# Kernel optimization log

Hardware: AMD Instinct MI355X
Metric: run time of the kernel (lower is better)

Reference implementation:

```python
import jax, jax.numpy as jnp
import numpy as np

DIM = 768
HEADS = 12
HEAD_DIM = DIM // HEADS
HIDDEN = 4 * DIM
EPS = 1e-5


def layernorm(x, g, b):
    mu = jnp.mean(x, axis=-1, keepdims=True)
    var = jnp.var(x, axis=-1, keepdims=True)
    return (x - mu) * jax.lax.rsqrt(var + EPS) * g + b


def setup_inputs() -> dict:
    key = jax.random.key(0)
    ks = jax.random.split(key, 16)
    s = 0.02
    return {
        "x_pre": jax.random.normal(ks[0], (8, 512, DIM), jnp.float32),
        "x_post": jax.random.normal(ks[1], (8, 512, DIM), jnp.float32),
        "attention_mask": jnp.zeros((8, 1, 1024, 1024), jnp.float32),
        "ln1_g": jnp.ones((DIM,), jnp.float32),
        "ln1_b": jnp.zeros((DIM,), jnp.float32),
        "Wq": jax.random.normal(ks[2], (DIM, DIM), jnp.float32) * s,
        "bq": jnp.zeros((DIM,), jnp.float32),
        "Wk": jax.random.normal(ks[3], (DIM, DIM), jnp.float32) * s,
        "bk": jnp.zeros((DIM,), jnp.float32),
        "Wv": jax.random.normal(ks[4], (DIM, DIM), jnp.float32) * s,
        "bv": jnp.zeros((DIM,), jnp.float32),
        "Wo": jax.random.normal(ks[5], (DIM, DIM), jnp.float32) * s,
        "bo": jnp.zeros((DIM,), jnp.float32),
        "ln2_g": jnp.ones((DIM,), jnp.float32),
        "ln2_b": jnp.zeros((DIM,), jnp.float32),
        "W1": jax.random.normal(ks[6], (DIM, HIDDEN), jnp.float32) * s,
        "b1": jnp.zeros((HIDDEN,), jnp.float32),
        "W2": jax.random.normal(ks[7], (HIDDEN, DIM), jnp.float32) * s,
        "b2": jnp.zeros((DIM,), jnp.float32),
        "gamma_1": 0.1 * jnp.ones((DIM,), jnp.float32),
        "gamma_2": 0.1 * jnp.ones((DIM,), jnp.float32),
    }


def reference(x_pre, x_post, attention_mask, ln1_g, ln1_b, Wq, bq, Wk, bk, Wv, bv,
              Wo, bo, ln2_g, ln2_b, W1, b1, W2, b2, gamma_1, gamma_2):
    x = jnp.concatenate((x_pre, x_post), axis=1)  # [B, N, C]
    B, N, C = x.shape
    h = layernorm(x, ln1_g, ln1_b)
    # self-attention with manual QK^T in float32
    q = (h @ Wq + bq).reshape(B, N, HEADS, HEAD_DIM)
    k = (h @ Wk + bk).reshape(B, N, HEADS, HEAD_DIM)
    v = (h @ Wv + bv).reshape(B, N, HEADS, HEAD_DIM)
    scale = HEAD_DIM ** -0.5
    attn = jnp.einsum("bqhd,bkhd->bhqk", q.astype(jnp.float32) * scale,
                      k.astype(jnp.float32)) + attention_mask
    attn = jax.nn.softmax(attn, axis=-1).astype(x.dtype)
    o = jnp.einsum("bhqk,bkhd->bqhd", attn, v).reshape(B, N, C)
    o = o @ Wo + bo
    x = x + gamma_1 * o
    # MLP
    h2 = layernorm(x, ln2_g, ln2_b)
    h2 = jax.nn.gelu(h2 @ W1 + b1, approximate=False) @ W2 + b2
    return x + gamma_2 * h2
```

## Files before the change

kernel.cpp:

```cpp
#include <hip/hip_runtime.h>
#include <hip/hip_fp8.h>
#include <cstdint>
#include <cstddef>

#define BATCH   8
#define SEQ     1024
#define DIMC    768
#define HEADS   12
#define HDIM    64
#define HIDDEN  3072
#define MROWS   (BATCH * SEQ)
#define L2E     1.4426950408889634f

typedef __attribute__((ext_vector_type(8))) short bf16x8;
typedef __attribute__((ext_vector_type(4))) float f32x4;

__device__ __forceinline__ unsigned short f2b(float f) {
    union { float f; unsigned int u; } v; v.f = f;
    unsigned int u = v.u;
    return (unsigned short)((u + 0x7FFFu + ((u >> 16) & 1u)) >> 16);
}
__device__ __forceinline__ unsigned char f2e4m3(float f) {
    __hip_fp8_e4m3 t(f); return t.__x;
}
__device__ __forceinline__ unsigned int b2u(float f) {
    union { float f; unsigned int u; } v; v.f = f; return v.u;
}
__device__ __forceinline__ float u2f(unsigned int u) {
    union { unsigned int u; float f; } v; v.u = u; return v.f;
}
__device__ __forceinline__ void gl_lds16(const void* g, void* l) {
    __builtin_amdgcn_global_load_lds(
        (const __attribute__((address_space(1))) unsigned int*)g,
        (__attribute__((address_space(3))) unsigned int*)l, 16, 0, 0);
}
__device__ __forceinline__ float gelu_fast(float x) {
    float p = x * x;
    float a = fmaf(p, 0.044715f, 1.0f);
    float w = x * a * -2.302118131f;
    float z = exp2f(w);
    return x * __builtin_amdgcn_rcpf(1.0f + z);
}

__global__ __launch_bounds__(256) void tcvt_k(const float* __restrict__ src,
                                              unsigned char* __restrict__ dst,
                                              int K, int N) {
    __shared__ float tile[32][33];
    int k0 = blockIdx.y * 32, n0 = blockIdx.x * 32;
    int tx = threadIdx.x, ty = threadIdx.y;
#pragma unroll
    for (int i = 0; i < 4; i++)
        tile[ty + i * 8][tx] = src[(size_t)(k0 + ty + i * 8) * N + n0 + tx];
    __syncthreads();
#pragma unroll
    for (int i = 0; i < 4; i++)
        dst[(size_t)(n0 + ty + i * 8) * K + k0 + tx] = f2e4m3(tile[tx][ty + i * 8]);
}

__global__ __launch_bounds__(256) void tcvt4_k(const float* __restrict__ s0,
                                               const float* __restrict__ s1,
                                               const float* __restrict__ s2,
                                               const float* __restrict__ s3,
                                               unsigned char* __restrict__ d0,
                                               unsigned char* __restrict__ d1,
                                               unsigned char* __restrict__ d2,
                                               unsigned char* __restrict__ d3) {
    const float* src = (blockIdx.z == 0) ? s0 : (blockIdx.z == 1) ? s1
                     : (blockIdx.z == 2) ? s2 : s3;
    unsigned char* dst = (blockIdx.z == 0) ? d0 : (blockIdx.z == 1) ? d1
                       : (blockIdx.z == 2) ? d2 : d3;
    __shared__ float tile[32][33];
    int k0 = blockIdx.y * 32, n0 = blockIdx.x * 32;
    int tx = threadIdx.x, ty = threadIdx.y;
#pragma unroll
    for (int i = 0; i < 4; i++)
        tile[ty + i * 8][tx] = src[(size_t)(k0 + ty + i * 8) * DIMC + n0 + tx];
    __syncthreads();
#pragma unroll
    for (int i = 0; i < 4; i++)
        dst[(size_t)(n0 + ty + i * 8) * DIMC + k0 + tx] = f2e4m3(tile[tx][ty + i * 8]);
}

__global__ __launch_bounds__(256) void vtr_k(const unsigned short* __restrict__ src,
                                             unsigned char* __restrict__ dst) {
    int bh = blockIdx.x, k0 = blockIdx.y * 64;
    __shared__ unsigned short t[64][68];
    const unsigned short* s = src + ((size_t)bh * SEQ + k0) * HDIM;
    unsigned char* d = dst + (size_t)bh * HDIM * SEQ + k0;
    int tid = threadIdx.x;
#pragma unroll
    for (int p = 0; p < 4; p++) {
        int c = p * 256 + tid;
        int key = c >> 4, dd = (c & 15) * 4;
        *(uint2*)&t[key][dd] = *(const uint2*)&s[key * HDIM + dd];
    }
    __syncthreads();
#pragma unroll
    for (int p = 0; p < 8; p++) {
        int idx = p * 256 + tid;
        int dd = idx >> 5, kk = (idx & 31) * 2;
        uchar2 o;
        o.x = f2e4m3(u2f((unsigned int)t[kk][dd] << 16));
        o.y = f2e4m3(u2f((unsigned int)t[kk + 1][dd] << 16));
        *(uchar2*)&d[(size_t)dd * SEQ + kk] = o;
    }
}

__global__ __launch_bounds__(256) void ln_k(const float* __restrict__ xa,
                                            const float* __restrict__ xb,
                                            const float* __restrict__ g,
                                            const float* __restrict__ bt,
                                            float* __restrict__ x_out,
                                            unsigned char* __restrict__ h_out) {
    int r = blockIdx.x;
    const float* src;
    if (xb) {
        int b = r >> 10, nn = r & 1023;
        src = (nn < 512) ? xa + ((size_t)b * 512 + nn) * DIMC
                         : xb + ((size_t)b * 512 + (nn - 512)) * DIMC;
    } else {
        src = xa + (size_t)r * DIMC;
    }
    int t = threadIdx.x;
    float v[3], s = 0.f, s2 = 0.f;
#pragma unroll
    for (int j = 0; j < 3; j++) {
        v[j] = src[t + j * 256];
        s += v[j]; s2 += v[j] * v[j];
    }
#pragma unroll
    for (int off = 32; off > 0; off >>= 1) {
        s  += __shfl_down(s,  off);
        s2 += __shfl_down(s2, off);
    }
    __shared__ float red[8];
    int wid = t >> 6, lane = t & 63;
    if (lane == 0) { red[wid] = s; red[4 + wid] = s2; }
    __syncthreads();
    s  = red[0] + red[1] + red[2] + red[3];
    s2 = red[4] + red[5] + red[6] + red[7];
    float mu  = s * (1.f / DIMC);
    float var = s2 * (1.f / DIMC) - mu * mu;
    float rstd = rsqrtf(var + 1e-5f);
#pragma unroll
    for (int j = 0; j < 3; j++) {
        int i = t + j * 256;
        float xv = v[j];
        if (x_out) x_out[(size_t)r * DIMC + i] = xv;
        h_out[(size_t)r * DIMC + i] = f2e4m3((xv - mu) * rstd * g[i] + bt[i]);
    }
}

template <int MODE, int TM>
__global__ __launch_bounds__(256) void gemm_k(
    const unsigned char* __restrict__ A,
    const unsigned char* __restrict__ Bt0,
    const unsigned char* __restrict__ Bt1,
    const unsigned char* __restrict__ Bt2,
    const float* __restrict__ bias0,
    const float* __restrict__ bias1,
    const float* __restrict__ bias2,
    const float* __restrict__ resid,
    const float* __restrict__ gamma,
    float* __restrict__ outf,
    unsigned short* __restrict__ outb0,
    unsigned short* __restrict__ outb1,
    unsigned short* __restrict__ outb2,
    unsigned char* __restrict__ outc,
    int K, int ldo) {

    constexpr int AI = TM / 32;
    const int tid  = threadIdx.x;
    const int wid  = tid >> 6, lane = tid & 63;
    const int quad = lane >> 4, l16 = lane & 15;
    const int m0 = blockIdx.y * TM, n0 = blockIdx.x * 128;
    const int waveM = (wid >> 1) * (AI * 16), waveN = (wid & 1) * 64;

    const unsigned char* Bt = Bt0;
    if (MODE == 0) Bt = (blockIdx.z == 0) ? Bt0 : (blockIdx.z == 1) ? Bt1 : Bt2;

    __shared__ __align__(16) unsigned char As[TM * 128];
    __shared__ __align__(16) unsigned char Bs[128 * 128];

    int carow[AI], caoff[AI], cbrow[4], cboff[4];
#pragma unroll
    for (int j = 0; j < AI; j++) {
        int c = j * 256 + tid;
        carow[j] = c >> 3;
        caoff[j] = ((c & 7) ^ (carow[j] & 7)) * 16;
    }
#pragma unroll
    for (int j = 0; j < 4; j++) {
        int c = j * 256 + tid;
        cbrow[j] = c >> 3;
        cboff[j] = ((c & 7) ^ (cbrow[j] & 7)) * 16;
    }
    const int asw = l16 & 7;
    int abase[AI], bbase[4];
#pragma unroll
    for (int i = 0; i < AI; i++)
        abase[i] = (waveM + i * 16 + l16) * 128 + (quad & 1) * 8;
#pragma unroll
    for (int i = 0; i < 4; i++)
        bbase[i] = (waveN + i * 16 + l16) * 128 + (quad & 1) * 8;

    f32x4 acc[AI][4] = {};

    for (int k0 = 0; k0 < K; k0 += 128) {
#pragma unroll
        for (int j = 0; j < AI; j++)
            gl_lds16(&A[(size_t)(m0 + carow[j]) * K + k0 + caoff[j]],
                     &As[(j * 256 + wid * 64) * 16]);
#pragma unroll
        for (int j = 0; j < 4; j++)
            gl_lds16(&Bt[(size_t)(n0 + cbrow[j]) * K + k0 + cboff[j]],
                     &Bs[(j * 256 + wid * 64) * 16]);
        __syncthreads();

#pragma unroll
        for (int kk = 0; kk < 4; kk++) {
            const int csw = ((kk * 2 + (quad >> 1)) ^ asw) * 16;
            long a[AI], b[4];
#pragma unroll
            for (int i = 0; i < AI; i++) a[i] = *(const long*)&As[abase[i] + csw];
#pragma unroll
            for (int i = 0; i < 4; i++) b[i] = *(const long*)&Bs[bbase[i] + csw];
#pragma unroll
            for (int i = 0; i < AI; i++)
#pragma unroll
                for (int j = 0; j < 4; j++)
                    acc[i][j] = __builtin_amdgcn_mfma_f32_16x16x32_fp8_fp8(
                        a[i], b[j], acc[i][j], 0, 0, 0);
        }
        __syncthreads();
    }

    const float* bias = bias0;
    unsigned short* outb = outb0;
    if (MODE == 0) {
        bias = (blockIdx.z == 0) ? bias0 : (blockIdx.z == 1) ? bias1 : bias2;
        outb = (blockIdx.z == 0) ? outb0 : (blockIdx.z == 1) ? outb1 : outb2;
    }
    const float qscale = 0.125f * L2E;
#pragma unroll
    for (int i = 0; i < AI; i++) {
#pragma unroll
        for (int j = 0; j < 4; j++) {
            int n = n0 + waveN + j * 16 + l16;
#pragma unroll
            for (int r = 0; r < 4; r++) {
                int m = m0 + waveM + i * 16 + quad * 4 + r;
                float val = acc[i][j][r];
                if (MODE == 0) {
                    val += bias[n];
                    if (blockIdx.z == 0) val *= qscale;
                    int bb = m >> 10, nn = m & 1023;
                    int hh = n >> 6,  d  = n & 63;
                    outb[(((size_t)bb * HEADS + hh) * SEQ + nn) * HDIM + d] = f2b(val);
                } else if (MODE == 1 || MODE == 3) {
                    val += bias[n];
                    outf[(size_t)m * ldo + n] =
                        resid[(size_t)m * ldo + n] + gamma[n] * val;
                } else {
                    outc[(size_t)m * ldo + n] = f2e4m3(gelu_fast(val + bias[n]));
                }
            }
        }
    }
}

__global__ __launch_bounds__(256) void attn_k(const unsigned short* __restrict__ Q,
                                              const unsigned short* __restrict__ Km,
                                              const unsigned char* __restrict__ Vt,
                                              const float* __restrict__ mask,
                                              unsigned char* __restrict__ O) {
    const int bh = blockIdx.x;
    const int b = bh / HEADS, h = bh - b * HEADS;
    const int tid = threadIdx.x;
    const int wid = tid >> 6, lane = tid & 63;
    const int quad = lane >> 4, l16 = lane & 15;
    const int qw = blockIdx.y * 64 + wid * 16;

    __shared__ __align__(16) unsigned short Ks[128 * 64];
    __shared__ __align__(16) unsigned char  Vs[64 * 128];
    __shared__ __align__(16) unsigned char  Ps[4][16 * 136];
    unsigned char* sp = Ps[wid];

    const unsigned short* Qp = Q + ((size_t)bh * SEQ + qw) * HDIM;
    bf16x8 aQ[2];
    aQ[0] = *(const bf16x8*)(Qp + l16 * HDIM + quad * 8);
    aQ[1] = *(const bf16x8*)(Qp + l16 * HDIM + 32 + quad * 8);

    int kql[4], vql[2];
#pragma unroll
    for (int j = 0; j < 4; j++) {
        int ck = (wid * 4 + j) * 64 + lane;
        int key = ck >> 3, ch = ck & 7;
        kql[j] = key * HDIM + ((ch ^ ((key >> 3) & 7)) * 8);
    }
#pragma unroll
    for (int j = 0; j < 2; j++) {
        int cv = j * 256 + wid * 64 + lane;
        int d = cv >> 3, ch = cv & 7;
        vql[j] = d * SEQ + ((ch ^ (d & 7)) * 16);
    }
    const unsigned short* Kb = Km + (size_t)bh * SEQ * HDIM;
    const unsigned char*  Vb = Vt + (size_t)bh * HDIM * SEQ;
    const float* Mbase = mask + (size_t)b * SEQ * SEQ
                       + (size_t)(qw + quad * 4) * SEQ + 8 * l16;

    f32x4 o[4] = {};
    f32x4 osum = {};
    const long ONES = 0x3838383838383838L;

    for (int key0 = 0; key0 < SEQ; key0 += 128) {
        float mreg[4][8];
        const float* mb = Mbase + key0;
#pragma unroll
        for (int r = 0; r < 4; r++) {
            float4 u0 = *(const float4*)(mb + r * SEQ);
            float4 u1 = *(const float4*)(mb + r * SEQ + 4);
            mreg[r][0] = u0.x; mreg[r][1] = u0.y; mreg[r][2] = u0.z; mreg[r][3] = u0.w;
            mreg[r][4] = u1.x; mreg[r][5] = u1.y; mreg[r][6] = u1.z; mreg[r][7] = u1.w;
        }
        const unsigned short* Kg = Kb + (size_t)key0 * HDIM;
        const unsigned char*  Vg = Vb + key0;
#pragma unroll
        for (int j = 0; j < 4; j++)
            gl_lds16(Kg + kql[j], &Ks[(wid * 4 + j) * 512]);
#pragma unroll
        for (int j = 0; j < 2; j++)
            gl_lds16(Vg + vql[j], &Vs[(j * 256 + wid * 64) * 16]);
        __syncthreads();

        f32x4 s[8];
#pragma unroll
        for (int nt = 0; nt < 8; nt++) {
            const unsigned short* kp = &Ks[(8 * l16 + nt) * 64];
            bf16x8 b0 = *(const bf16x8*)&kp[(quad ^ (l16 & 7)) * 8];
            bf16x8 b1 = *(const bf16x8*)&kp[((4 + quad) ^ (l16 & 7)) * 8];
            f32x4 t = {};
            t = __builtin_amdgcn_mfma_f32_16x16x32_bf16(aQ[0], b0, t, 0, 0, 0);
            t = __builtin_amdgcn_mfma_f32_16x16x32_bf16(aQ[1], b1, t, 0, 0, 0);
            s[nt] = t;
        }

#pragma unroll
        for (int r = 0; r < 4; r++) {
            float e[8];
#pragma unroll
            for (int nt = 0; nt < 8; nt++)
                e[nt] = exp2f(fmaf(mreg[r][nt], L2E, s[nt][r]));
            unsigned int d0 = __builtin_amdgcn_cvt_pk_fp8_f32(e[0], e[1], 0, false);
            d0 = __builtin_amdgcn_cvt_pk_fp8_f32(e[2], e[3], d0, true);
            unsigned int d1 = __builtin_amdgcn_cvt_pk_fp8_f32(e[4], e[5], 0, false);
            d1 = __builtin_amdgcn_cvt_pk_fp8_f32(e[6], e[7], d1, true);
            int prow = quad * 4 + r;
            uint2 pv; pv.x = d0; pv.y = d1;
            *(uint2*)&sp[prow * 136 + ((l16 ^ (prow & 7)) * 8)] = pv;
        }
        __builtin_amdgcn_wave_barrier();

        long aP[4];
#pragma unroll
        for (int kt = 0; kt < 4; kt++)
            aP[kt] = *(const long*)&sp[l16 * 136 + (((kt * 4 + quad) ^ (l16 & 7)) * 8)];
#pragma unroll
        for (int kt = 0; kt < 4; kt++)
            osum = __builtin_amdgcn_mfma_f32_16x16x32_fp8_fp8(aP[kt], ONES, osum, 0, 0, 0);
#pragma unroll
        for (int dt = 0; dt < 4; dt++) {
            const unsigned char* vp = &Vs[(dt * 16 + l16) * 128];
            f32x4 oo = o[dt];
#pragma unroll
            for (int kt = 0; kt < 4; kt++) {
                long bv = *(const long*)
                    &vp[(((kt * 2 + (quad >> 1)) ^ (l16 & 7)) * 16) + (quad & 1) * 8];
                oo = __builtin_amdgcn_mfma_f32_16x16x32_fp8_fp8(aP[kt], bv, oo, 0, 0, 0);
            }
            o[dt] = oo;
        }
        __syncthreads();
    }

#pragma unroll
    for (int r = 0; r < 4; r++) {
        float inv = 1.0f / osum[r];
#pragma unroll
        for (int dt = 0; dt < 4; dt++)
            O[(size_t)(b * SEQ + qw + quad * 4 + r) * DIMC + h * HDIM + dt * 16 + l16] =
                f2e4m3(o[dt][r] * inv);
    }
}

extern "C" void kernel_launch(void* const* d_in, const int* in_sizes, int n_in,
                              void* d_out, int out_size, void* d_ws, size_t ws_size,
                              hipStream_t stream) {
    const float* x_pre = (const float*)d_in[0];
    const float* x_post= (const float*)d_in[1];
    const float* mask  = (const float*)d_in[2];
    const float* ln1g  = (const float*)d_in[3];
    const float* ln1b  = (const float*)d_in[4];
    const float* Wq    = (const float*)d_in[5];
    const float* bq    = (const float*)d_in[6];
    const float* Wk    = (const float*)d_in[7];
    const float* bk    = (const float*)d_in[8];
    const float* Wv    = (const float*)d_in[9];
    const float* bv    = (const float*)d_in[10];
    const float* Wo    = (const float*)d_in[11];
    const float* bo    = (const float*)d_in[12];
    const float* ln2g  = (const float*)d_in[13];
    const float* ln2b  = (const float*)d_in[14];
    const float* W1    = (const float*)d_in[15];
    const float* b1    = (const float*)d_in[16];
    const float* W2    = (const float*)d_in[17];
    const float* b2    = (const float*)d_in[18];
    const float* g1    = (const float*)d_in[19];
    const float* g2    = (const float*)d_in[20];
    float* out = (float*)d_out;

    char* p = (char*)d_ws;
    float* xf  = (float*)p;                  p += (size_t)MROWS * DIMC * 4;
    float* x2f = (float*)p;                  p += (size_t)MROWS * DIMC * 4;
    unsigned char* h8  = (unsigned char*)p;  p += (size_t)MROWS * DIMC;
    unsigned char* O8  = (unsigned char*)p;  p += (size_t)MROWS * DIMC;
    unsigned char* G8  = (unsigned char*)p;  p += (size_t)MROWS * HIDDEN;
    unsigned short* Qb = (unsigned short*)p; p += (size_t)MROWS * DIMC * 2;
    unsigned short* Kb = (unsigned short*)p; p += (size_t)MROWS * DIMC * 2;
    unsigned short* Vb = (unsigned short*)p; p += (size_t)MROWS * DIMC * 2;
    unsigned char* V8  = (unsigned char*)p;  p += (size_t)MROWS * DIMC;
    unsigned char* Wq8 = (unsigned char*)p;  p += (size_t)DIMC * DIMC;
    unsigned char* Wk8 = (unsigned char*)p;  p += (size_t)DIMC * DIMC;
    unsigned char* Wv8 = (unsigned char*)p;  p += (size_t)DIMC * DIMC;
    unsigned char* Wo8 = (unsigned char*)p;  p += (size_t)DIMC * DIMC;
    unsigned char* W18 = (unsigned char*)p;  p += (size_t)DIMC * HIDDEN;
    unsigned char* W28 = (unsigned char*)p;  p += (size_t)DIMC * HIDDEN;

    dim3 tb(32, 8);
    tcvt4_k<<<dim3(24, 24, 4), tb, 0, stream>>>(Wq, Wk, Wv, Wo, Wq8, Wk8, Wv8, Wo8);
    tcvt_k<<<dim3(96, 24), tb, 0, stream>>>(W1, W18, DIMC, HIDDEN);
    tcvt_k<<<dim3(24, 96), tb, 0, stream>>>(W2, W28, HIDDEN, DIMC);

    ln_k<<<MROWS, 256, 0, stream>>>(x_pre, x_post, ln1g, ln1b, xf, h8);

    gemm_k<0, 128><<<dim3(6, 64, 3), 256, 0, stream>>>(h8, Wq8, Wk8, Wv8,
        bq, bk, bv, nullptr, nullptr, nullptr, Qb, Kb, Vb, nullptr, DIMC, DIMC);

    vtr_k<<<dim3(96, 16), 256, 0, stream>>>(Vb, V8);

    attn_k<<<dim3(96, 16), 256, 0, stream>>>(Qb, Kb, V8, mask, O8);

    gemm_k<1, 64><<<dim3(6, 128), 256, 0, stream>>>(O8, Wo8, nullptr, nullptr,
        bo, nullptr, nullptr, xf, g1, x2f, nullptr, nullptr, nullptr, nullptr, DIMC, DIMC);

    ln_k<<<MROWS, 256, 0, stream>>>(x2f, nullptr, ln2g, ln2b, nullptr, h8);

    gemm_k<2, 128><<<dim3(24, 64), 256, 0, stream>>>(h8, W18, nullptr, nullptr,
        b1, nullptr, nullptr, nullptr, nullptr, nullptr, nullptr, nullptr, nullptr,
        G8, DIMC, HIDDEN);

    gemm_k<3, 64><<<dim3(6, 128), 256, 0, stream>>>(G8, W28, nullptr, nullptr,
        b2, nullptr, nullptr, x2f, g2, out, nullptr, nullptr, nullptr, nullptr,
        HIDDEN, DIMC);

    (void)in_sizes; (void)n_in; (void)out_size; (void)ws_size;
}
```

Measured before the change: 381.4 us.

## Merge weight conversions, fuse V transpose into QKV GEMM, remap attention blocks

Folds the three weight-conversion launches into one flat-indexed kernel. The QKV GEMM epilogue now writes V straight to the transposed fp8 layout, which removes the separate bf16 V buffer and the transpose kernel. Attention blocks are remapped so each XCD handles one batch for L2 locality, and s_setprio is raised around the MFMA sections. The fused V epilogue writes 4-byte scattered stores with stride SEQ, which may coalesce poorly.

Measured after the change: 366.8 us. 3.8% less time.

```diff
diff --git a/kernel.cpp b/kernel.cpp
--- a/kernel.cpp
+++ b/kernel.cpp
@@ -42,11 +42,34 @@
     return x * __builtin_amdgcn_rcpf(1.0f + z);
 }
 
-__global__ __launch_bounds__(256) void tcvt_k(const float* __restrict__ src,
-                                              unsigned char* __restrict__ dst,
-                                              int K, int N) {
+__global__ __launch_bounds__(256) void tcvt_all(
+    const float* __restrict__ s0, const float* __restrict__ s1,
+    const float* __restrict__ s2, const float* __restrict__ s3,
+    const float* __restrict__ s4, const float* __restrict__ s5,
+    unsigned char* __restrict__ d0, unsigned char* __restrict__ d1,
+    unsigned char* __restrict__ d2, unsigned char* __restrict__ d3,
+    unsigned char* __restrict__ d4, unsigned char* __restrict__ d5) {
     __shared__ float tile[32][33];
-    int k0 = blockIdx.y * 32, n0 = blockIdx.x * 32;
+    int id = blockIdx.x;
+    const float* src; unsigned char* dst;
+    int K, N, k0, n0;
+    if (id < 2304) {
+        int mat = id / 576, rem = id % 576;
+        K = 768; N = 768;
+        k0 = (rem / 24) * 32; n0 = (rem % 24) * 32;
+        src = (mat == 0) ? s0 : (mat == 1) ? s1 : (mat == 2) ? s2 : s3;
+        dst = (mat == 0) ? d0 : (mat == 1) ? d1 : (mat == 2) ? d2 : d3;
+    } else if (id < 4608) {
+        int rem = id - 2304;
+        K = 768; N = 3072;
+        k0 = (rem / 96) * 32; n0 = (rem % 96) * 32;
+        src = s4; dst = d4;
+    } else {
+        int rem = id - 4608;
+        K = 3072; N = 768;
+        k0 = (rem / 24) * 32; n0 = (rem % 24) * 32;
+        src = s5; dst = d5;
+    }
     int tx = threadIdx.x, ty = threadIdx.y;
 #pragma unroll
     for (int i = 0; i < 4; i++)
@@ -55,55 +78,6 @@
 #pragma unroll
     for (int i = 0; i < 4; i++)
         dst[(size_t)(n0 + ty + i * 8) * K + k0 + tx] = f2e4m3(tile[tx][ty + i * 8]);
-}
-
-__global__ __launch_bounds__(256) void tcvt4_k(const float* __restrict__ s0,
-                                               const float* __restrict__ s1,
-                                               const float* __restrict__ s2,
-                                               const float* __restrict__ s3,
-                                               unsigned char* __restrict__ d0,
-                                               unsigned char* __restrict__ d1,
-                                               unsigned char* __restrict__ d2,
-                                               unsigned char* __restrict__ d3) {
-    const float* src = (blockIdx.z == 0) ? s0 : (blockIdx.z == 1) ? s1
-                     : (blockIdx.z == 2) ? s2 : s3;
-    unsigned char* dst = (blockIdx.z == 0) ? d0 : (blockIdx.z == 1) ? d1
-                       : (blockIdx.z == 2) ? d2 : d3;
-    __shared__ float tile[32][33];
-    int k0 = blockIdx.y * 32, n0 = blockIdx.x * 32;
-    int tx = threadIdx.x, ty = threadIdx.y;
-#pragma unroll
-    for (int i = 0; i < 4; i++)
-        tile[ty + i * 8][tx] = src[(size_t)(k0 + ty + i * 8) * DIMC + n0 + tx];
-    __syncthreads();
-#pragma unroll
-    for (int i = 0; i < 4; i++)
-        dst[(size_t)(n0 + ty + i * 8) * DIMC + k0 + tx] = f2e4m3(tile[tx][ty + i * 8]);
-}
-
-__global__ __launch_bounds__(256) void vtr_k(const unsigned short* __restrict__ src,
-                                             unsigned char* __restrict__ dst) {
-    int bh = blockIdx.x, k0 = blockIdx.y * 64;
-    __shared__ unsigned short t[64][68];
-    const unsigned short* s = src + ((size_t)bh * SEQ + k0) * HDIM;
-    unsigned char* d = dst + (size_t)bh * HDIM * SEQ + k0;
-    int tid = threadIdx.x;
-#pragma unroll
-    for (int p = 0; p < 4; p++) {
-        int c = p * 256 + tid;
-        int key = c >> 4, dd = (c & 15) * 4;
-        *(uint2*)&t[key][dd] = *(const uint2*)&s[key * HDIM + dd];
-    }
-    __syncthreads();
-#pragma unroll
-    for (int p = 0; p < 8; p++) {
-        int idx = p * 256 + tid;
-        int dd = idx >> 5, kk = (idx & 31) * 2;
-        uchar2 o;
-        o.x = f2e4m3(u2f((unsigned int)t[kk][dd] << 16));
-        o.y = f2e4m3(u2f((unsigned int)t[kk + 1][dd] << 16));
-        *(uchar2*)&d[(size_t)dd * SEQ + kk] = o;
-    }
 }
 
 __global__ __launch_bounds__(256) void ln_k(const float* __restrict__ xa,
@@ -247,6 +221,19 @@
 #pragma unroll
         for (int j = 0; j < 4; j++) {
             int n = n0 + waveN + j * 16 + l16;
+            if (MODE == 0 && blockIdx.z == 2) {
+                int hh = n >> 6, d = n & 63;
+                float bn = bias[n];
+                int mb = m0 + waveM + i * 16 + quad * 4;
+                int bb = mb >> 10, nn = mb & 1023;
+                unsigned int packed = 0;
+#pragma unroll
+                for (int r = 0; r < 4; r++)
+                    packed |= (unsigned int)f2e4m3(acc[i][j][r] + bn) << (8 * r);
+                *(unsigned int*)&outc[(((size_t)bb * HEADS + hh) * HDIM + d) * SEQ + nn]
+                    = packed;
+                continue;
+            }
 #pragma unroll
             for (int r = 0; r < 4; r++) {
                 int m = m0 + waveM + i * 16 + quad * 4 + r;
@@ -274,12 +261,15 @@
                                               const unsigned char* __restrict__ Vt,
                                               const float* __restrict__ mask,
                                               unsigned char* __restrict__ O) {
-    const int bh = blockIdx.x;
-    const int b = bh / HEADS, h = bh - b * HEADS;
+    const int flat = blockIdx.y * 96 + blockIdx.x;
+    const int xcd  = flat & 7, slot = flat >> 3;
+    const int h = slot % 12, y = slot / 12;
+    const int b = xcd;
+    const int bh = b * HEADS + h;
     const int tid = threadIdx.x;
     const int wid = tid >> 6, lane = tid & 63;
     const int quad = lane >> 4, l16 = lane & 15;
-    const int qw = blockIdx.y * 64 + wid * 16;
+    const int qw = y * 64 + wid * 16;
 
     __shared__ __align__(16) unsigned short Ks[128 * 64];
     __shared__ __align__(16) unsigned char  Vs[64 * 128];
@@ -334,6 +324,7 @@
         __syncthreads();
 
         f32x4 s[8];
+        __builtin_amdgcn_s_setprio(1);
 #pragma unroll
         for (int nt = 0; nt < 8; nt++) {
             const unsigned short* kp = &Ks[(8 * l16 + nt) * 64];
@@ -344,6 +335,7 @@
             t = __builtin_amdgcn_mfma_f32_16x16x32_bf16(aQ[1], b1, t, 0, 0, 0);
             s[nt] = t;
         }
+        __builtin_amdgcn_s_setprio(0);
 
 #pragma unroll
         for (int r = 0; r < 4; r++) {
@@ -365,6 +357,7 @@
 #pragma unroll
         for (int kt = 0; kt < 4; kt++)
             aP[kt] = *(const long*)&sp[l16 * 136 + (((kt * 4 + quad) ^ (l16 & 7)) * 8)];
+        __builtin_amdgcn_s_setprio(1);
 #pragma unroll
         for (int kt = 0; kt < 4; kt++)
             osum = __builtin_amdgcn_mfma_f32_16x16x32_fp8_fp8(aP[kt], ONES, osum, 0, 0, 0);
@@ -380,6 +373,7 @@
             }
             o[dt] = oo;
         }
+        __builtin_amdgcn_s_setprio(0);
         __syncthreads();
     }
 
@@ -427,7 +421,6 @@
     unsigned char* G8  = (unsigned char*)p;  p += (size_t)MROWS * HIDDEN;
     unsigned short* Qb = (unsigned short*)p; p += (size_t)MROWS * DIMC * 2;
     unsigned short* Kb = (unsigned short*)p; p += (size_t)MROWS * DIMC * 2;
-    unsigned short* Vb = (unsigned short*)p; p += (size_t)MROWS * DIMC * 2;
     unsigned char* V8  = (unsigned char*)p;  p += (size_t)MROWS * DIMC;
     unsigned char* Wq8 = (unsigned char*)p;  p += (size_t)DIMC * DIMC;
     unsigned char* Wk8 = (unsigned char*)p;  p += (size_t)DIMC * DIMC;
@@ -437,16 +430,13 @@
     unsigned char* W28 = (unsigned char*)p;  p += (size_t)DIMC * HIDDEN;
 
     dim3 tb(32, 8);
-    tcvt4_k<<<dim3(24, 24, 4), tb, 0, stream>>>(Wq, Wk, Wv, Wo, Wq8, Wk8, Wv8, Wo8);
-    tcvt_k<<<dim3(96, 24), tb, 0, stream>>>(W1, W18, DIMC, HIDDEN);
-    tcvt_k<<<dim3(24, 96), tb, 0, stream>>>(W2, W28, HIDDEN, DIMC);
+    tcvt_all<<<6912, tb, 0, stream>>>(Wq, Wk, Wv, Wo, W1, W2,
+                                      Wq8, Wk8, Wv8, Wo8, W18, W28);
 
     ln_k<<<MROWS, 256, 0, stream>>>(x_pre, x_post, ln1g, ln1b, xf, h8);
 
     gemm_k<0, 128><<<dim3(6, 64, 3), 256, 0, stream>>>(h8, Wq8, Wk8, Wv8,
-        bq, bk, bv, nullptr, nullptr, nullptr, Qb, Kb, Vb, nullptr, DIMC, DIMC);
-
-    vtr_k<<<dim3(96, 16), 256, 0, stream>>>(Vb, V8);
+        bq, bk, bv, nullptr, nullptr, nullptr, Qb, Kb, nullptr, V8, DIMC, DIMC);
 
     attn_k<<<dim3(96, 16), 256, 0, stream>>>(Qb, Kb, V8, mask, O8);
 
```
